# Kernel tuning notes

Hardware: AMD Instinct MI355X
Metric: run time of the kernel (lower is better)

## Reference

```python
import jax, jax.numpy as jnp
import numpy as np

B, N, D, H = 8, 1024, 768, 12
HD = D // H  # head_dim = 64


def setup_inputs() -> dict:
    key = jax.random.key(0)
    ks = jax.random.split(key, 7)
    s = 1.0 / np.sqrt(D)  # xavier-ish scale for weights
    return {
        "x1": jax.random.normal(ks[0], (B, N, D), dtype=jnp.float32),
        "x2": jax.random.normal(ks[1], (B, N, D), dtype=jnp.float32),
        "Wq": jax.random.normal(ks[2], (D, D), dtype=jnp.float32) * s,
        "Wk": jax.random.normal(ks[3], (D, D), dtype=jnp.float32) * s,
        "Wv": jax.random.normal(ks[4], (D, D), dtype=jnp.float32) * s,
        "Wo": jax.random.normal(ks[5], (D, D), dtype=jnp.float32) * s,
        "bo": jnp.zeros((D,), dtype=jnp.float32),
    }


def _heads(x):
    # (B, N, D) -> (B, H, N, HD)
    return x.reshape(B, -1, H, HD).transpose(0, 2, 1, 3)


def reference(x1, x2, Wq, Wk, Wv, Wo, bo):
    scale = 1.0 / jnp.sqrt(jnp.asarray(HD, x1.dtype))
    q1 = _heads(x1 @ Wq.T)               # (B,H,N,HD)
    k1 = _heads(x1 @ Wk.T)
    v1 = _heads(x1 @ Wv.T)
    k2 = _heads(x2 @ Wk.T)
    v2 = _heads(x2 @ Wv.T)
    kc = jnp.concatenate([k1, k2], axis=2)   # (B,H,2N,HD)
    vc = jnp.concatenate([v1, v2], axis=2)
    attn = jnp.einsum('bhnd,bhmd->bhnm', q1, kc) * scale  # (B,H,N,2N)
    attn = jax.nn.softmax(attn, axis=-1)
    out = jnp.einsum('bhnm,bhmd->bhnd', attn, vc)          # (B,H,N,HD)
    out = out.transpose(0, 2, 1, 3).reshape(B, N, D)
    return out @ Wo.T + bo
```

## Files before the change

kernel.cpp:

```cpp
#include <hip/hip_runtime.h>


typedef __bf16 bf16x8 __attribute__((ext_vector_type(8)));
typedef float  f32x4  __attribute__((ext_vector_type(4)));
typedef unsigned int u32x4 __attribute__((ext_vector_type(4)));
typedef short  s16x4  __attribute__((ext_vector_type(4)));

__device__ __forceinline__ unsigned short bf16bits(float f) {
    return __builtin_bit_cast(unsigned short, (__bf16)f);
}
__device__ __forceinline__ unsigned pk2(float a, float b) {
    return (unsigned)bf16bits(a) | ((unsigned)bf16bits(b) << 16);
}
__device__ __forceinline__ bf16x8 asbf(u32x4 v) {
    return __builtin_bit_cast(bf16x8, v);
}
__device__ __forceinline__ float fexp2(float x) {
#if __has_builtin(__builtin_amdgcn_exp2f)
    return __builtin_amdgcn_exp2f(x);
#else
    return exp2f(x);
#endif
}
__device__ __forceinline__ float frcp(float x) {
#if __has_builtin(__builtin_amdgcn_rcpf)
    return __builtin_amdgcn_rcpf(x);
#else
    return 1.0f / x;
#endif
}

#define MFMA32(a, b, c) __builtin_amdgcn_mfma_f32_16x16x32_bf16((a), (b), (c), 0, 0, 0)
#define AS1(p) (const __attribute__((address_space(1))) void*)(p)
#define AS3(p) (__attribute__((address_space(3))) void*)(p)

__global__ __launch_bounds__(256) void convert_all(
    const float* __restrict__ x1, const float* __restrict__ x2,
    const float* __restrict__ Wq, const float* __restrict__ Wk,
    const float* __restrict__ Wv, const float* __restrict__ Wo,
    unsigned short* __restrict__ x1b, unsigned short* __restrict__ x2b,
    unsigned short* __restrict__ Wcat, unsigned short* __restrict__ Wob)
{
    const float* src; unsigned short* dst; int n4;
    switch (blockIdx.y) {
        case 0:  src = x1; dst = x1b;            n4 = 1572864; break;
        case 1:  src = x2; dst = x2b;            n4 = 1572864; break;
        case 2:  src = Wq; dst = Wcat;           n4 = 147456;  break;
        case 3:  src = Wk; dst = Wcat +  589824; n4 = 147456;  break;
        case 4:  src = Wv; dst = Wcat + 1179648; n4 = 147456;  break;
        default: src = Wo; dst = Wob;            n4 = 147456;  break;
    }
    int i = blockIdx.x * 256 + threadIdx.x;
    if (i >= n4) return;
    float4 v = ((const float4*)src)[i];
    unsigned* o32 = (unsigned*)(dst + (size_t)i * 4);
    o32[0] = pk2(v.x, v.y);
    o32[1] = pk2(v.z, v.w);
}

__global__ __launch_bounds__(512, 2) void gemm256(
    const unsigned short* __restrict__ A1, const unsigned short* __restrict__ A2,
    const unsigned short* __restrict__ Wcat,
    unsigned short* __restrict__ dQ, unsigned short* __restrict__ dK,
    unsigned short* __restrict__ dV)
{
    __shared__ u32x4 smA[2][2048];
    __shared__ u32x4 smB[2][2048];

    const int tid  = threadIdx.x;
    const int lane = tid & 63;
    const int l15  = lane & 15;
    const int g    = lane >> 4;
    const int wid  = tid >> 6;
    const int wm   = wid >> 2;
    const int wn   = wid & 3;
    const int rb   = blockIdx.x;
    const int jb   = blockIdx.y;

    const bool br2 = (jb >= 9);
    const unsigned short* A  = br2 ? A2 : A1;
    const unsigned short* Bw = br2 ? (Wcat + 589824) : Wcat;
    const int jcol = br2 ? (jb - 9) : jb;

    f32x4 acc[8][4] = {};

#define STG_A(KT, BUF, MH, K)                                                        \
    {                                                                                \
        int s_  = wn * 64 + (K) * 256 + lane;   \
        int rl_ = s_ >> 3, ps_ = s_ & 7;                                             \
        const unsigned short* src_ = A +                                             \
            (size_t)(rb * 256 + wm * 128 + (MH) * 64 + rl_) * 768 +                  \
            (KT) * 64 + (ps_ ^ (rl_ & 7)) * 8;                                       \
        __builtin_amdgcn_global_load_lds(AS1(src_),                                  \
            AS3(&smA[BUF][wm * 1024 + (MH) * 512 + wn * 64 + (K) * 256]), 16, 0, 0); \
    }
#define STG_B(KT, BUF, K)                                                            \
    {                                                                                \
        int s_  = wm * 64 + (K) * 128 + lane;    \
        int rl_ = s_ >> 3, ps_ = s_ & 7;                                             \
        const unsigned short* src_ = Bw +                                            \
            (size_t)(jcol * 256 + wn * 64 + rl_) * 768 +                             \
            (KT) * 64 + (ps_ ^ (rl_ & 7)) * 8;                                       \
        __builtin_amdgcn_global_load_lds(AS1(src_),                                  \
            AS3(&smB[BUF][wn * 512 + wm * 64 + (K) * 128]), 16, 0, 0);               \
    }

    STG_A(0, 0, 0, 0) STG_A(0, 0, 0, 1)
    STG_B(0, 0, 0) STG_B(0, 0, 1) STG_B(0, 0, 2) STG_B(0, 0, 3)
    STG_A(0, 0, 1, 0) STG_A(0, 0, 1, 1)
    asm volatile("s_waitcnt vmcnt(0)" ::: "memory");
    __builtin_amdgcn_s_barrier();

    for (int kt = 0; kt < 12; ++kt) {
        const int buf = kt & 1;
        const int nb  = buf ^ 1;
        const bool st = (kt < 11);
        const u32x4* bA = smA[buf];
        const u32x4* bB = smB[buf];
        bf16x8 af[4], bfr[4];

#pragma unroll
        for (int n = 0; n < 4; ++n) {
            int row = wn * 64 + n * 16 + l15;
            bfr[n] = asbf(bB[row * 8 + (g ^ (row & 7))]);
        }
#pragma unroll
        for (int m = 0; m < 4; ++m) {
            int row = wm * 128 + m * 16 + l15;
            af[m] = asbf(bA[row * 8 + (g ^ (row & 7))]);
        }
        if (st) { STG_A(kt + 1, nb, 0, 0) STG_A(kt + 1, nb, 0, 1) }
        if (kt == 11) { asm volatile("s_waitcnt vmcnt(0)" ::: "memory"); }
        else          { asm volatile("s_waitcnt vmcnt(2)" ::: "memory"); }
        __builtin_amdgcn_sched_barrier(0);
        __builtin_amdgcn_s_barrier();
        __builtin_amdgcn_sched_barrier(0);
        __builtin_amdgcn_s_setprio(1);
#pragma unroll
        for (int m = 0; m < 4; ++m)
#pragma unroll
            for (int n = 0; n < 4; ++n)
                acc[m][n] = MFMA32(af[m], bfr[n], acc[m][n]);
        __builtin_amdgcn_s_setprio(0);

#pragma unroll
        for (int m = 0; m < 4; ++m) {
            int row = wm * 128 + 64 + m * 16 + l15;
            af[m] = asbf(bA[row * 8 + (g ^ (row & 7))]);
        }
        if (st) { STG_B(kt + 1, nb, 0) STG_B(kt + 1, nb, 1) }
        __builtin_amdgcn_sched_barrier(0);
        __builtin_amdgcn_s_barrier();
        __builtin_amdgcn_sched_barrier(0);
        __builtin_amdgcn_s_setprio(1);
#pragma unroll
        for (int m = 0; m < 4; ++m)
#pragma unroll
            for (int n = 0; n < 4; ++n)
                acc[4 + m][n] = MFMA32(af[m], bfr[n], acc[4 + m][n]);
        __builtin_amdgcn_s_setprio(0);

#pragma unroll
        for (int n = 0; n < 4; ++n) {
            int row = wn * 64 + n * 16 + l15;
            bfr[n] = asbf(bB[row * 8 + ((4 + g) ^ (row & 7))]);
        }
#pragma unroll
        for (int m = 0; m < 4; ++m) {
            int row = wm * 128 + m * 16 + l15;
            af[m] = asbf(bA[row * 8 + ((4 + g) ^ (row & 7))]);
        }
        if (st) { STG_B(kt + 1, nb, 2) STG_B(kt + 1, nb, 3) }
        __builtin_amdgcn_sched_barrier(0);
        __builtin_amdgcn_s_barrier();
        __builtin_amdgcn_sched_barrier(0);
        __builtin_amdgcn_s_setprio(1);
#pragma unroll
        for (int m = 0; m < 4; ++m)
#pragma unroll
            for (int n = 0; n < 4; ++n)
                acc[m][n] = MFMA32(af[m], bfr[n], acc[m][n]);
        __builtin_amdgcn_s_setprio(0);

#pragma unroll
        for (int m = 0; m < 4; ++m) {
            int row = wm * 128 + 64 + m * 16 + l15;
            af[m] = asbf(bA[row * 8 + ((4 + g) ^ (row & 7))]);
        }
        if (st) { STG_A(kt + 1, nb, 1, 0) STG_A(kt + 1, nb, 1, 1) }
        if (st) { asm volatile("s_waitcnt vmcnt(2)" ::: "memory"); }
        __builtin_amdgcn_sched_barrier(0);
        __builtin_amdgcn_s_barrier();
        __builtin_amdgcn_sched_barrier(0);
        __builtin_amdgcn_s_setprio(1);
#pragma unroll
        for (int m = 0; m < 4; ++m)
#pragma unroll
            for (int n = 0; n < 4; ++n)
                acc[4 + m][n] = MFMA32(af[m], bfr[n], acc[4 + m][n]);
        __builtin_amdgcn_s_setprio(0);
    }
#undef STG_A
#undef STG_B

    const int rloc = wm * 128 + g * 4;
    const int cloc = wn * 64 + l15;
    const int seg  = jcol / 3;
    const int segq = br2 ? seg + 3 : seg;
    const int cseg = (jcol - seg * 3) * 256;
#pragma unroll
    for (int mf = 0; mf < 8; ++mf) {
#pragma unroll
        for (int n = 0; n < 4; ++n) {
            int r0 = rb * 256 + rloc + mf * 16;
            int cl = cseg + cloc + n * 16;
            int b = r0 >> 10, nn = r0 & 1023;
            int h = cl >> 6, hd = cl & 63;
            if (segq == 0) {
#pragma unroll
                for (int reg = 0; reg < 4; ++reg)
                    dQ[((size_t)(b * 12 + h) * 1024 + nn + reg) * 64 + hd] =
                        bf16bits(acc[mf][n][reg] * 0.18033688f);
            } else if (segq == 1 || segq == 3) {
                size_t koff = (segq == 3) ? 1024 : 0;
#pragma unroll
                for (int reg = 0; reg < 4; ++reg)
                    dK[((size_t)(b * 12 + h) * 2048 + koff + nn + reg) * 64 + hd] =
                        bf16bits(acc[mf][n][reg]);
            } else {
                size_t koff = (segq == 4) ? 1024 : 0;
                uint2 w;
                w.x = pk2(acc[mf][n][0], acc[mf][n][1]);
                w.y = pk2(acc[mf][n][2], acc[mf][n][3]);
                *(uint2*)(dV + ((size_t)(b * 12 + h) * 64 + hd) * 2048 +
                          koff + nn) = w;
            }
        }
    }
}

__global__ __launch_bounds__(256) void gemm_out(
    const unsigned short* __restrict__ A, const unsigned short* __restrict__ Bw,
    float* __restrict__ dO, const float* __restrict__ bias)
{
    __shared__ u32x4 smA[2048];
    __shared__ u32x4 smB[2048];

    const int tid  = threadIdx.x;
    const int lane = tid & 63;
    const int l15  = lane & 15;
    const int g    = lane >> 4;
    const int wid  = tid >> 6;
    const int rb   = blockIdx.x;
    const int jb   = blockIdx.y;
    const int wr   = (wid >> 1) * 64;
    const int wc   = (wid & 1) * 64;

    f32x4 acc[4][4] = {};

#define GSTAGE(KT, BO)                                                               \
    {                                                                                \
        int kt_ = (KT);                                                              \
        _Pragma("unroll")                                                            \
        for (int c_ = 0; c_ < 4; ++c_) {                                             \
            int i_   = (wid + c_ * 4) * 64 + lane;                                   \
            int row_ = i_ >> 3;                                                      \
            int gs_  = (i_ & 7) ^ (row_ & 7);                                        \
            const unsigned short* sa = A +                                           \
                (size_t)(rb * 128 + row_) * 768 + kt_ * 64 + gs_ * 8;                \
            __builtin_amdgcn_global_load_lds(AS1(sa),                                \
                AS3(smA + (BO) + (wid + c_ * 4) * 64), 16, 0, 0);                    \
            const unsigned short* sb = Bw +                                          \
                (size_t)(jb * 128 + row_) * 768 + kt_ * 64 + gs_ * 8;                \
            __builtin_amdgcn_global_load_lds(AS1(sb),                                \
                AS3(smB + (BO) + (wid + c_ * 4) * 64), 16, 0, 0);                    \
        }                                                                            \
    }

    GSTAGE(0, 0)

    for (int kt = 0; kt < 12; ++kt) {
        __builtin_amdgcn_s_barrier();
        if (kt < 11) {
            GSTAGE(kt + 1, ((kt + 1) & 1) << 10)
            asm volatile("s_waitcnt vmcnt(8)" ::: "memory");
        } else {
            asm volatile("s_waitcnt vmcnt(0)" ::: "memory");
        }
        __builtin_amdgcn_s_barrier();
        __builtin_amdgcn_sched_barrier(0);

        const u32x4* bA = smA + ((kt & 1) << 10);
        const u32x4* bB = smB + ((kt & 1) << 10);

#pragma unroll
        for (int kk = 0; kk < 2; ++kk) {
            bf16x8 af[4], bfr[4];
#pragma unroll
            for (int m = 0; m < 4; ++m) {
                int row = wr + m * 16 + l15;
                af[m] = asbf(bA[row * 8 + ((kk * 4 + g) ^ (row & 7))]);
            }
#pragma unroll
            for (int n = 0; n < 4; ++n) {
                int row = wc + n * 16 + l15;
                bfr[n] = asbf(bB[row * 8 + ((kk * 4 + g) ^ (row & 7))]);
            }
#pragma unroll
            for (int m = 0; m < 4; ++m)
#pragma unroll
                for (int n = 0; n < 4; ++n)
                    acc[m][n] = MFMA32(af[m], bfr[n], acc[m][n]);
        }
    }
#undef GSTAGE

    const int rloc = wr + g * 4;
    const int cloc = wc + l15;
#pragma unroll
    for (int m = 0; m < 4; ++m)
#pragma unroll
        for (int n = 0; n < 4; ++n) {
            int r0 = rb * 128 + rloc + m * 16;
            int c  = jb * 128 + cloc + n * 16;
#pragma unroll
            for (int reg = 0; reg < 4; ++reg)
                dO[(size_t)(r0 + reg) * 768 + c] = acc[m][n][reg] + bias[c];
        }
}

__global__ __launch_bounds__(256, 3) void attn_k(
    const unsigned short* __restrict__ Q, const unsigned short* __restrict__ K,
    const unsigned short* __restrict__ Vt, unsigned short* __restrict__ AO)
{
    __shared__ u32x4 sK[1536];
    __shared__ u32x4 sV[1536];

    const int tid  = threadIdx.x;
    const int lane = tid & 63;
    const int g    = lane >> 4;
    const int l15  = lane & 15;
    const int wid  = tid >> 6;
    const int qh   = wid & 1;
    const int kvh  = wid >> 1;
    const int bh   = blockIdx.x;
    const int q0   = blockIdx.y * 128;

    const unsigned short* Qh = Q  + (size_t)bh * (1024 * 64);
    const unsigned short* Kh = K  + (size_t)bh * (2048 * 64);
    const unsigned short* Vh = Vt + (size_t)bh * (64 * 2048);

    bf16x8 qf[4][2];
#pragma unroll
    for (int m = 0; m < 4; ++m)
#pragma unroll
        for (int kk = 0; kk < 2; ++kk)
            qf[m][kk] = *(const bf16x8*)(Qh +
                (size_t)(q0 + qh * 64 + m * 16 + l15) * 64 + kk * 32 + g * 8);

    f32x4 o[4][4] = {};
    float lr[4] = {0.f, 0.f, 0.f, 0.f};

#define STAGE_TILE(T, DOFF)                                                          \
    {                                                                                \
        int t_ = (T);                                                                \
        _Pragma("unroll")                                                            \
        for (int c_ = 0; c_ < 2; ++c_) {                                             \
            int i_   = (wid + c_ * 4) * 64 + lane;                                   \
            int row_ = i_ >> 3;                                                      \
            int gsK_ = (i_ & 7) ^ ((row_ & 3) | ((row_ >> 1) & 4));                  \
            int gsV_ = (i_ & 7) ^ (row_ & 7);                                        \
            const unsigned short* srcK_ = Kh + ((size_t)t_ * 64 + row_) * 64 + gsK_ * 8; \
            __builtin_amdgcn_global_load_lds(AS1(srcK_),                             \
                AS3(sK + (DOFF) + (wid + c_ * 4) * 64), 16, 0, 0);                   \
            const unsigned short* srcV_ = Vh + (size_t)row_ * 2048 + t_ * 64 + gsV_ * 8; \
            __builtin_amdgcn_global_load_lds(AS1(srcV_),                             \
                AS3(sV + (DOFF) + (wid + c_ * 4) * 64), 16, 0, 0);                   \
        }                                                                            \
    }

    STAGE_TILE(0, 0)
    STAGE_TILE(1, 512)

    for (int t = 0; t < 32; ++t) {
        if (t < 31) { asm volatile("s_waitcnt vmcnt(4)" ::: "memory"); }
        else        { asm volatile("s_waitcnt vmcnt(0)" ::: "memory"); }
        __builtin_amdgcn_s_barrier();
        if (t < 30) {
            STAGE_TILE(t + 2, ((t + 2) % 3) * 512)
        }
        __builtin_amdgcn_sched_barrier(0);

        const u32x4* sKb = sK + (t % 3) * 512;
        const u32x4* sVb = sV + (t % 3) * 512;

        f32x4 s[2][4] = {};
        __builtin_amdgcn_s_setprio(1);
#pragma unroll
        for (int kk = 0; kk < 2; ++kk) {
            bf16x8 kf[2];
#pragma unroll
            for (int j = 0; j < 2; ++j) {
                int rowp = (kvh << 5) + ((l15 >> 2) << 3) + (j << 2) + (l15 & 3);
                kf[j] = asbf(sKb[rowp * 8 + ((kk * 4 + g) ^ (l15 & 7))]);
            }
#pragma unroll
            for (int j = 0; j < 2; ++j)
#pragma unroll
                for (int m = 0; m < 4; ++m)
                    s[j][m] = MFMA32(kf[j], qf[m][kk], s[j][m]);
        }
        __builtin_amdgcn_s_setprio(0);

        s16x4 p16[2][4];
#pragma unroll
        for (int m = 0; m < 4; ++m) {
            float p0 = fexp2(s[0][m][0]), p1 = fexp2(s[0][m][1]);
            float p2 = fexp2(s[0][m][2]), p3 = fexp2(s[0][m][3]);
            float p4 = fexp2(s[1][m][0]), p5 = fexp2(s[1][m][1]);
            float p6 = fexp2(s[1][m][2]), p7 = fexp2(s[1][m][3]);
            lr[m] += (p0 + p1) + (p2 + p3) + (p4 + p5) + (p6 + p7);
            p16[0][m] = (s16x4){ (short)bf16bits(p0), (short)bf16bits(p1),
                                 (short)bf16bits(p2), (short)bf16bits(p3) };
            p16[1][m] = (s16x4){ (short)bf16bits(p4), (short)bf16bits(p5),
                                 (short)bf16bits(p6), (short)bf16bits(p7) };
        }

        __builtin_amdgcn_s_setprio(1);
        bf16x8 pf[4];
#pragma unroll
        for (int m = 0; m < 4; ++m)
            pf[m] = __builtin_bit_cast(bf16x8,
                __builtin_shufflevector(p16[0][m], p16[1][m],
                                        0, 1, 2, 3, 4, 5, 6, 7));
#pragma unroll
        for (int v = 0; v < 4; ++v) {
            int row = v * 16 + l15;
            bf16x8 vf = asbf(sVb[row * 8 + ((kvh * 4 + g) ^ (row & 7))]);
#pragma unroll
            for (int m = 0; m < 4; ++m)
                o[v][m] = MFMA32(vf, pf[m], o[v][m]);
        }
        __builtin_amdgcn_s_setprio(0);
    }

#pragma unroll
    for (int m = 0; m < 4; ++m) {
        lr[m] += __shfl_xor(lr[m], 16);
        lr[m] += __shfl_xor(lr[m], 32);
    }
    __syncthreads();

    float* oK   = (float*)sK;
    float* oVf  = (float*)sV;
    float* obuf = qh ? oVf : oK;
    float* lbuf = oVf + 64 * 72;

    if (kvh == 1) {
#pragma unroll
        for (int m = 0; m < 4; ++m)
#pragma unroll
            for (int v = 0; v < 4; ++v)
                *(f32x4*)&obuf[(m * 16 + l15) * 72 + v * 16 + g * 4] = o[v][m];
        if (lane < 16) {
#pragma unroll
            for (int m = 0; m < 4; ++m)
                lbuf[qh * 64 + m * 16 + l15] = lr[m];
        }
    }
    __syncthreads();

    if (kvh == 0) {
        const int b = bh / 12, h = bh % 12;
#pragma unroll
        for (int m = 0; m < 4; ++m) {
            float lt = lr[m] + lbuf[qh * 64 + m * 16 + l15];
            float rl = frcp(lt);
            int q = q0 + qh * 64 + m * 16 + l15;
            unsigned short* dst = AO + (size_t)(b * 1024 + q) * 768 + h * 64 + g * 4;
#pragma unroll
            for (int v = 0; v < 4; ++v) {
                f32x4 add = *(const f32x4*)&obuf[(m * 16 + l15) * 72 + v * 16 + g * 4];
                uint2 w;
                w.x = pk2((o[v][m][0] + add[0]) * rl, (o[v][m][1] + add[1]) * rl);
                w.y = pk2((o[v][m][2] + add[2]) * rl, (o[v][m][3] + add[3]) * rl);
                *(uint2*)(dst + v * 16) = w;
            }
        }
    }
#undef STAGE_TILE
}

extern "C" void kernel_launch(void* const* d_in, const int* in_sizes, int n_in,
                              void* d_out, int out_size, void* d_ws, size_t ws_size,
                              hipStream_t stream)
{
    const float* x1 = (const float*)d_in[0];
    const float* x2 = (const float*)d_in[1];
    const float* Wq = (const float*)d_in[2];
    const float* Wk = (const float*)d_in[3];
    const float* Wv = (const float*)d_in[4];
    const float* Wo = (const float*)d_in[5];
    const float* bo = (const float*)d_in[6];

    unsigned short* Wcat = (unsigned short*)d_ws;
    unsigned short* Wob  = Wcat + 1769472;
    unsigned short* x1b  = Wob  + 589824;
    unsigned short* x2b  = x1b  + 6291456;
    unsigned short* Qb   = x2b  + 6291456;
    unsigned short* Kc   = Qb   + 6291456;
    unsigned short* Vt   = Kc   + 12582912;
    unsigned short* AO   = x1b;

    convert_all<<<dim3(6144, 6), 256, 0, stream>>>(x1, x2, Wq, Wk, Wv, Wo,
                                                   x1b, x2b, Wcat, Wob);

    gemm256<<<dim3(32, 15), 512, 0, stream>>>(x1b, x2b, Wcat, Qb, Kc, Vt);

    attn_k<<<dim3(96, 8), 256, 0, stream>>>(Qb, Kc, Vt, AO);

    gemm_out<<<dim3(64, 6), 256, 0, stream>>>(AO, Wob, (float*)d_out, bo);
}
```

Before: 150.1 us.

## Software-pipeline attention loop: overlap PV of previous tile with QK of current

Restructures the attention inner loop so the P·V MFMAs for tile t-1 are issued right after the Q·K MFMAs for tile t, while the exp2/softmax of tile t follows. V staging is split from K staging and runs one tile behind, with an epilogue doing the last PV product. The aim is to interleave transcendental (exp) work with matrix-core work and hide its latency. The cost is extra live registers for the carried P fragments and more complex wait-count bookkeeping.

```diff
diff --git a/kernel.cpp b/kernel.cpp
--- a/kernel.cpp
+++ b/kernel.cpp
@@ -86,7 +86,7 @@
 
 #define STG_A(KT, BUF, MH, K)                                                        \
     {                                                                                \
-        int s_  = wn * 64 + (K) * 256 + lane;   \
+        int s_  = wn * 64 + (K) * 256 + lane;                                        \
         int rl_ = s_ >> 3, ps_ = s_ & 7;                                             \
         const unsigned short* src_ = A +                                             \
             (size_t)(rb * 256 + wm * 128 + (MH) * 64 + rl_) * 768 +                  \
@@ -96,7 +96,7 @@
     }
 #define STG_B(KT, BUF, K)                                                            \
     {                                                                                \
-        int s_  = wm * 64 + (K) * 128 + lane;    \
+        int s_  = wm * 64 + (K) * 128 + lane;                                        \
         int rl_ = s_ >> 3, ps_ = s_ & 7;                                             \
         const unsigned short* src_ = Bw +                                            \
             (size_t)(jcol * 256 + wn * 64 + rl_) * 768 +                             \
@@ -360,8 +360,9 @@
 
     f32x4 o[4][4] = {};
     float lr[4] = {0.f, 0.f, 0.f, 0.f};
-
-#define STAGE_TILE(T, DOFF)                                                          \
+    bf16x8 pfp[4];
+
+#define STAGE_K(T, DOFF)                                                             \
     {                                                                                \
         int t_ = (T);                                                                \
         _Pragma("unroll")                                                            \
@@ -369,30 +370,38 @@
             int i_   = (wid + c_ * 4) * 64 + lane;                                   \
             int row_ = i_ >> 3;                                                      \
             int gsK_ = (i_ & 7) ^ ((row_ & 3) | ((row_ >> 1) & 4));                  \
-            int gsV_ = (i_ & 7) ^ (row_ & 7);                                        \
             const unsigned short* srcK_ = Kh + ((size_t)t_ * 64 + row_) * 64 + gsK_ * 8; \
             __builtin_amdgcn_global_load_lds(AS1(srcK_),                             \
                 AS3(sK + (DOFF) + (wid + c_ * 4) * 64), 16, 0, 0);                   \
+        }                                                                            \
+    }
+#define STAGE_V(T, DOFF)                                                             \
+    {                                                                                \
+        int t_ = (T);                                                                \
+        _Pragma("unroll")                                                            \
+        for (int c_ = 0; c_ < 2; ++c_) {                                             \
+            int i_   = (wid + c_ * 4) * 64 + lane;                                   \
+            int row_ = i_ >> 3;                                                      \
+            int gsV_ = (i_ & 7) ^ (row_ & 7);                                        \
             const unsigned short* srcV_ = Vh + (size_t)row_ * 2048 + t_ * 64 + gsV_ * 8; \
             __builtin_amdgcn_global_load_lds(AS1(srcV_),                             \
                 AS3(sV + (DOFF) + (wid + c_ * 4) * 64), 16, 0, 0);                   \
         }                                                                            \
     }
 
-    STAGE_TILE(0, 0)
-    STAGE_TILE(1, 512)
+    STAGE_K(0, 0)
+    STAGE_V(0, 0)
+    STAGE_K(1, 512)
 
     for (int t = 0; t < 32; ++t) {
         if (t < 31) { asm volatile("s_waitcnt vmcnt(4)" ::: "memory"); }
-        else        { asm volatile("s_waitcnt vmcnt(0)" ::: "memory"); }
-        __builtin_amdgcn_s_barrier();
-        if (t < 30) {
-            STAGE_TILE(t + 2, ((t + 2) % 3) * 512)
-        }
+        else        { asm volatile("s_waitcnt vmcnt(2)" ::: "memory"); }
+        __builtin_amdgcn_s_barrier();
+        if (t < 30) STAGE_K(t + 2, ((t + 2) % 3) * 512)
+        if (t < 31) STAGE_V(t + 1, ((t + 1) % 3) * 512)
         __builtin_amdgcn_sched_barrier(0);
 
         const u32x4* sKb = sK + (t % 3) * 512;
-        const u32x4* sVb = sV + (t % 3) * 512;
 
         f32x4 s[2][4] = {};
         __builtin_amdgcn_s_setprio(1);
@@ -410,9 +419,20 @@
                 for (int m = 0; m < 4; ++m)
                     s[j][m] = MFMA32(kf[j], qf[m][kk], s[j][m]);
         }
+        if (t > 0) {
+            const u32x4* sVbp = sV + ((t + 2) % 3) * 512;
+#pragma unroll
+            for (int v = 0; v < 4; ++v) {
+                int row = v * 16 + l15;
+                bf16x8 vf = asbf(sVbp[row * 8 + ((kvh * 4 + g) ^ (row & 7))]);
+#pragma unroll
+                for (int m = 0; m < 4; ++m)
+                    o[v][m] = MFMA32(vf, pfp[m], o[v][m]);
+            }
+        }
         __builtin_amdgcn_s_setprio(0);
-
-        s16x4 p16[2][4];
+        __builtin_amdgcn_sched_barrier(0);
+
 #pragma unroll
         for (int m = 0; m < 4; ++m) {
             float p0 = fexp2(s[0][m][0]), p1 = fexp2(s[0][m][1]);
@@ -420,26 +440,27 @@
             float p4 = fexp2(s[1][m][0]), p5 = fexp2(s[1][m][1]);
             float p6 = fexp2(s[1][m][2]), p7 = fexp2(s[1][m][3]);
             lr[m] += (p0 + p1) + (p2 + p3) + (p4 + p5) + (p6 + p7);
-            p16[0][m] = (s16x4){ (short)bf16bits(p0), (short)bf16bits(p1),
-                                 (short)bf16bits(p2), (short)bf16bits(p3) };
-            p16[1][m] = (s16x4){ (short)bf16bits(p4), (short)bf16bits(p5),
-                                 (short)bf16bits(p6), (short)bf16bits(p7) };
-        }
-
+            s16x4 a = (s16x4){ (short)bf16bits(p0), (short)bf16bits(p1),
+                               (short)bf16bits(p2), (short)bf16bits(p3) };
+            s16x4 b = (s16x4){ (short)bf16bits(p4), (short)bf16bits(p5),
+                               (short)bf16bits(p6), (short)bf16bits(p7) };
+            pfp[m] = __builtin_bit_cast(bf16x8,
+                __builtin_shufflevector(a, b, 0, 1, 2, 3, 4, 5, 6, 7));
+        }
+    }
+
+    asm volatile("s_waitcnt vmcnt(0)" ::: "memory");
+    __builtin_amdgcn_s_barrier();
+    {
+        const u32x4* sVbp = sV + (31 % 3) * 512;
         __builtin_amdgcn_s_setprio(1);
-        bf16x8 pf[4];
-#pragma unroll
-        for (int m = 0; m < 4; ++m)
-            pf[m] = __builtin_bit_cast(bf16x8,
-                __builtin_shufflevector(p16[0][m], p16[1][m],
-                                        0, 1, 2, 3, 4, 5, 6, 7));
 #pragma unroll
         for (int v = 0; v < 4; ++v) {
             int row = v * 16 + l15;
-            bf16x8 vf = asbf(sVb[row * 8 + ((kvh * 4 + g) ^ (row & 7))]);
+            bf16x8 vf = asbf(sVbp[row * 8 + ((kvh * 4 + g) ^ (row & 7))]);
 #pragma unroll
             for (int m = 0; m < 4; ++m)
-                o[v][m] = MFMA32(vf, pf[m], o[v][m]);
+                o[v][m] = MFMA32(vf, pfp[m], o[v][m]);
         }
         __builtin_amdgcn_s_setprio(0);
     }
@@ -488,7 +509,8 @@
             }
         }
     }
-#undef STAGE_TILE
+#undef STAGE_K
+#undef STAGE_V
 }
 
 extern "C" void kernel_launch(void* const* d_in, const int* in_sizes, int n_in,
```

Result: slower. 165.9 us (+10.5%).
